# Optimization experiments

Measured on AMD Instinct MI355X. Metric: run time of the kernel, lower is better.

The kernel has to match this reference:

```python
import jax, jax.numpy as jnp
import numpy as np
import math


def setup_inputs() -> dict:
    key = jax.random.key(0)
    k0, k1, k2, k3, k4 = jax.random.split(key, 5)
    in_f, out_f, nb = 512, 512, 8
    B, S = 4, 2048
    x = jax.random.normal(k0, (B, S, in_f), dtype=jnp.float32)
    # RBF params (frozen in original: basis_trainable=False)
    fan_in = in_f  # fan_in of rbf.weight.T which is (num_basis, in_features)
    bound = 1.0 / math.sqrt(fan_in)
    rbf_weight = jax.random.uniform(k1, (in_f, nb), dtype=jnp.float32,
                                    minval=-math.sqrt(3.0) * 0.33 / math.sqrt(fan_in),
                                    maxval=math.sqrt(3.0) * 0.33 / math.sqrt(fan_in))
    rbf_centers = jnp.tile(jnp.linspace(-bound, bound, nb, dtype=jnp.float32)[None, :], (in_f, 1))
    # KAN spline weight (in, nb, out); fan_in for init is in_f*nb
    fan2 = in_f * nb
    wb = math.sqrt(3.0) * 0.33 / math.sqrt(fan2)
    weight = jax.random.uniform(k2, (in_f, nb, out_f), dtype=jnp.float32, minval=-wb, maxval=wb)
    bias = jax.random.uniform(k3, (out_f,), dtype=jnp.float32,
                              minval=-1.0 / math.sqrt(fan2), maxval=1.0 / math.sqrt(fan2))
    scale_base = jax.random.uniform(k4, (in_f, out_f), dtype=jnp.float32, minval=-0.1, maxval=0.1)
    return {"x": x, "rbf_weight": rbf_weight, "rbf_centers": rbf_centers,
            "weight": weight, "bias": bias, "scale_base": scale_base}


def reference(x, rbf_weight, rbf_centers, weight, bias, scale_base):
    in_f = x.shape[-1]
    nb = rbf_weight.shape[1]
    beta = (nb / math.log2(nb)) ** 2  # get_rbf_width(2/nb, log2(nb))
    batch_shape = x.shape[:-1]
    xf = x.reshape(-1, in_f)  # (N, in)
    # RBF basis expansion: (N, in, nb)
    z = xf[:, :, None] * rbf_weight[None, :, :] - rbf_centers[None, :, :]
    phi = jnp.exp(-beta * (z * z))
    # spline contraction + base path, expressed as efficient contractions
    y = jnp.einsum('nib,ibo->no', phi, weight)
    y = y + bias + jnp.cos(xf) @ scale_base
    return y.reshape(*batch_shape, weight.shape[-1])
```

## Files before the change

### kernel.cpp

```cpp
#include <hip/hip_runtime.h>
#include <hip/hip_bf16.h>

typedef __attribute__((ext_vector_type(8))) short short8;
typedef __attribute__((ext_vector_type(4))) float f32x4;

#define IN_F 512
#define OUT_F 512
#define BK 64
#define PHI_STEPS 64
#define NSTEPS 72
#define PAN 64
#define ACH 512
#define BCH2 2048
#define NT2 2
#define PART_ELEMS (8192 * OUT_F)
#define C2 (-10.2591705f)

__device__ __forceinline__ short f2bf(float f) {
  unsigned u = __builtin_bit_cast(unsigned, f);
  u += 0x7fffu + ((u >> 16) & 1u);
  return (short)(u >> 16);
}
__device__ __forceinline__ float b2f(unsigned short u) {
  return __builtin_bit_cast(float, (unsigned)u << 16);
}

__device__ __forceinline__ void glds16(const void* g, void* l) {
  __builtin_amdgcn_global_load_lds(
      (const __attribute__((address_space(1))) unsigned int*)g,
      (__attribute__((address_space(3))) unsigned int*)l, 16, 0, 0);
}

__device__ __forceinline__ float bsrc(const float* __restrict__ w,
                                      const float* __restrict__ sb,
                                      int k, int col) {
  return (k < IN_F * 8) ? w[(size_t)k * OUT_F + col]
                        : sb[(size_t)(k - IN_F * 8) * OUT_F + col];
}

__global__ void __launch_bounds__(256) prep_b2(const float* __restrict__ w,
                                               const float* __restrict__ sb,
                                               short* __restrict__ img) {
  const int D = blockIdx.x * 256 + threadIdx.x;
  const int ci = D & (BCH2 - 1);
  const int im = D >> 11;
  const int s = im % NSTEPS;
  const int nt = im / NSTEPS;
  const int n = ci >> 3, slot = ci & 7;
  const int oct = slot ^ (n & 7);
  const int col = nt * 256 + n;
  short8 v;
#pragma unroll
  for (int j = 0; j < 8; ++j) v[j] = f2bf(bsrc(w, sb, s * 64 + oct * 8 + j, col));
  *(short8*)&img[(size_t)D * 8] = v;
}

__global__ void __launch_bounds__(256) prep_a(const float* __restrict__ x,
                                              const float* __restrict__ rw,
                                              const float* __restrict__ rc,
                                              short* __restrict__ aimg) {
  const int D = blockIdx.x * 256 + threadIdx.x;
  const int ci = D & (ACH - 1);
  const int rest = D >> 9;
  const int s = rest % NSTEPS;
  const int pan = rest / NSTEPS;
  const int m = ci >> 3, slot = ci & 7;
  const int oct = slot ^ (m & 7);
  const int row = pan * PAN + m;
  short8 v;
  if (s < PHI_STEPS) {
    const int feat = s * 8 + oct;
    const float xv = x[(size_t)row * IN_F + feat];
    const float4 r0 = *(const float4*)(rw + feat * 8);
    const float4 r1 = *(const float4*)(rw + feat * 8 + 4);
    const float4 q0 = *(const float4*)(rc + feat * 8);
    const float4 q1 = *(const float4*)(rc + feat * 8 + 4);
    const float rwv[8] = {r0.x, r0.y, r0.z, r0.w, r1.x, r1.y, r1.z, r1.w};
    const float rcv[8] = {q0.x, q0.y, q0.z, q0.w, q1.x, q1.y, q1.z, q1.w};
#pragma unroll
    for (int j = 0; j < 8; ++j) {
      const float z = fmaf(xv, rwv[j], -rcv[j]);
      v[j] = f2bf(exp2f(C2 * z * z));
    }
  } else {
    const float* xp = x + (size_t)row * IN_F + (s - PHI_STEPS) * 64 + oct * 8;
    const float4 u0 = *(const float4*)xp, u1 = *(const float4*)(xp + 4);
    v[0] = f2bf(__cosf(u0.x)); v[1] = f2bf(__cosf(u0.y));
    v[2] = f2bf(__cosf(u0.z)); v[3] = f2bf(__cosf(u0.w));
    v[4] = f2bf(__cosf(u1.x)); v[5] = f2bf(__cosf(u1.y));
    v[6] = f2bf(__cosf(u1.z)); v[7] = f2bf(__cosf(u1.w));
  }
  *(short8*)&aimg[(size_t)D * 8] = v;
}

__global__ void __launch_bounds__(256) reduce3b(const short* __restrict__ part,
                                                float* __restrict__ out) {
  typedef __attribute__((ext_vector_type(4))) short short4v;
  const int n4 = PART_ELEMS / 4;
  const short4v* p0 = (const short4v*)part;
  const short4v* p1 = (const short4v*)(part + PART_ELEMS);
  const short4v* p2 = (const short4v*)(part + 2 * (size_t)PART_ELEMS);
  float4* o4 = (float4*)out;
  for (int i = blockIdx.x * 256 + threadIdx.x; i < n4; i += gridDim.x * 256) {
    float4 a = o4[i];
    const short4v q0 = p0[i], q1 = p1[i], q2 = p2[i];
    a.x += b2f((unsigned short)q0[0]) + b2f((unsigned short)q1[0]) + b2f((unsigned short)q2[0]);
    a.y += b2f((unsigned short)q0[1]) + b2f((unsigned short)q1[1]) + b2f((unsigned short)q2[1]);
    a.z += b2f((unsigned short)q0[2]) + b2f((unsigned short)q1[2]) + b2f((unsigned short)q2[2]);
    a.w += b2f((unsigned short)q0[3]) + b2f((unsigned short)q1[3]) + b2f((unsigned short)q2[3]);
    o4[i] = a;
  }
}

__global__ void __launch_bounds__(256) reduce_add(const float* __restrict__ part,
                                                  float* __restrict__ out) {
  const int n4 = PART_ELEMS / 4;
  const float4* p4 = (const float4*)part;
  float4* o4 = (float4*)out;
  for (int i = blockIdx.x * 256 + threadIdx.x; i < n4; i += gridDim.x * 256) {
    float4 a = o4[i];
    const float4 b = p4[i];
    a.x += b.x; a.y += b.y; a.z += b.z; a.w += b.w;
    o4[i] = a;
  }
}

__global__ void __launch_bounds__(1024, 4) kan_gemm256(
    const short* __restrict__ aimg, const short* __restrict__ bimg,
    const float* __restrict__ bias, float* __restrict__ out,
    short* __restrict__ part) {
  constexpr int SPLC = NSTEPS / 4;
  __shared__ __align__(16) short A_lds[2][256 * BK];
  __shared__ __align__(16) short B_lds[2][256 * BK];

  const int t = threadIdx.x, lane = t & 63, wid = t >> 6;
  const int wm = wid >> 2, wn = wid & 3;
  const int l15 = lane & 15, kb = lane >> 4;
  const int mb = blockIdx.x, nt = blockIdx.y;
  const int ks = blockIdx.z;
  const int m0 = mb * 256, n0 = nt * 256, s0 = ks * SPLC;

  f32x4 acc[4][4];
#pragma unroll
  for (int i = 0; i < 4; ++i)
#pragma unroll
    for (int j = 0; j < 4; ++j) acc[i][j] = (f32x4){0.f, 0.f, 0.f, 0.f};

  auto stage = [&](int s, int buf) {
#pragma unroll
    for (int c = 0; c < 2; ++c) {
      const int g = c * 1024 + t;
      const int p = g >> 9, idx = g & 511;
      const short* src = aimg + (((size_t)(4 * mb + p) * NSTEPS + s) * ACH + idx) * 8;
      glds16(src, &A_lds[buf][c * 8192 + wid * 512]);
    }
#pragma unroll
    for (int c = 0; c < 2; ++c) {
      const int g = c * 1024 + t;
      const short* src = bimg + (((size_t)nt * NSTEPS + s) * BCH2 + g) * 8;
      glds16(src, &B_lds[buf][c * 8192 + wid * 512]);
    }
  };

  auto mfma_step = [&](int buf) {
#pragma unroll
    for (int kk = 0; kk < 2; ++kk) {
      const int sk = kk * 4 + kb;
      short8 af[4], bf[4];
#pragma unroll
      for (int mi = 0; mi < 4; ++mi) {
        const int rm = mi * 16 + l15;
        af[mi] = *(const short8*)&A_lds[buf][wm * 4096 + rm * 64 + (sk ^ (rm & 7)) * 8];
      }
#pragma unroll
      for (int ni = 0; ni < 4; ++ni) {
        const int n = wn * 64 + ni * 16 + l15;
        bf[ni] = *(const short8*)&B_lds[buf][n * 64 + (sk ^ (n & 7)) * 8];
      }
#pragma unroll
      for (int mi = 0; mi < 4; ++mi)
#pragma unroll
        for (int ni = 0; ni < 4; ++ni)
          acc[mi][ni] = __builtin_amdgcn_mfma_f32_16x16x32_bf16(
              af[mi], bf[ni], acc[mi][ni], 0, 0, 0);
    }
  };

  stage(s0, 0);

  for (int si = 0; si < SPLC; ++si) {
    const int c = si & 1;
    if (si + 1 < SPLC) {
      stage(s0 + si + 1, c ^ 1);
      asm volatile("s_waitcnt vmcnt(4)" ::: "memory");
    } else {
      asm volatile("s_waitcnt vmcnt(0)" ::: "memory");
    }
    __builtin_amdgcn_s_barrier();
    mfma_step(c);
    __builtin_amdgcn_s_barrier();
  }

#pragma unroll
  for (int ni = 0; ni < 4; ++ni) {
    const int col = n0 + wn * 64 + ni * 16 + l15;
    const float bb = (ks == 0) ? bias[col] : 0.f;
#pragma unroll
    for (int mi = 0; mi < 4; ++mi) {
      const int rb = m0 + wm * 64 + mi * 16 + kb * 4;
#pragma unroll
      for (int r4 = 0; r4 < 4; ++r4) {
        const size_t idx = (size_t)(rb + r4) * OUT_F + col;
        if (ks == 0) out[idx] = acc[mi][ni][r4] + bb;
        else         part[(size_t)(ks - 1) * PART_ELEMS + idx] = f2bf(acc[mi][ni][r4]);
      }
    }
  }
}

template <int KS>
__global__ void __launch_bounds__(512, 4) kan_gemm_mid(
    const short* __restrict__ aimg, const short* __restrict__ bimg,
    const float* __restrict__ bias, float* __restrict__ out,
    float* __restrict__ part) {
  constexpr int SPLC = NSTEPS / KS;
  __shared__ __align__(16) short A_lds[2][64 * BK];
  __shared__ __align__(16) short B_lds[2][256 * BK];

  const int t = threadIdx.x, lane = t & 63, wid = t >> 6;
  const int wm = wid >> 2, wn = wid & 3;
  const int l15 = lane & 15, kb = lane >> 4;
  const int mb = blockIdx.x, nt = blockIdx.y;
  const int ks = (KS > 1) ? blockIdx.z : 0;
  const int m0 = mb * 64, n0 = nt * 256, s0 = ks * SPLC;

  f32x4 acc[2][4];
#pragma unroll
  for (int i = 0; i < 2; ++i)
#pragma unroll
    for (int j = 0; j < 4; ++j) acc[i][j] = (f32x4){0.f, 0.f, 0.f, 0.f};

  const short* abase = aimg + (size_t)mb * NSTEPS * ACH * 8;
  const short* bbase = bimg + (size_t)nt * NSTEPS * BCH2 * 8;

  auto stage = [&](int s, int buf) {
    const short* as = abase + ((size_t)s * ACH + wid * 64 + lane) * 8;
    glds16(as, &A_lds[buf][wid * 512]);
    const short* bs = bbase + ((size_t)s * BCH2 + wid * 64 + lane) * 8;
#pragma unroll
    for (int c2 = 0; c2 < 4; ++c2)
      glds16(bs + (size_t)c2 * 512 * 8, &B_lds[buf][c2 * 4096 + wid * 512]);
  };

  auto mfma_step = [&](int buf) {
#pragma unroll
    for (int kk = 0; kk < 2; ++kk) {
      const int sk = kk * 4 + kb;
      short8 af[2], bf[4];
#pragma unroll
      for (int mi = 0; mi < 2; ++mi) {
        const int r = wm * 32 + mi * 16 + l15;
        af[mi] = *(const short8*)&A_lds[buf][r * BK + (sk ^ (r & 7)) * 8];
      }
#pragma unroll
      for (int ni = 0; ni < 4; ++ni) {
        const int n = wn * 64 + ni * 16 + l15;
        bf[ni] = *(const short8*)&B_lds[buf][n * BK + (sk ^ (n & 7)) * 8];
      }
#pragma unroll
      for (int mi = 0; mi < 2; ++mi)
#pragma unroll
        for (int ni = 0; ni < 4; ++ni)
          acc[mi][ni] = __builtin_amdgcn_mfma_f32_16x16x32_bf16(
              af[mi], bf[ni], acc[mi][ni], 0, 0, 0);
    }
  };

  stage(s0, 0);
  for (int si = 0; si < SPLC; ++si) {
    const int c = si & 1;
    if (si + 1 < SPLC) {
      stage(s0 + si + 1, c ^ 1);
      asm volatile("s_waitcnt vmcnt(5)" ::: "memory");
    } else {
      asm volatile("s_waitcnt vmcnt(0)" ::: "memory");
    }
    __builtin_amdgcn_s_barrier();
    mfma_step(c);
    __builtin_amdgcn_s_barrier();
  }

#pragma unroll
  for (int ni = 0; ni < 4; ++ni) {
    const int col = n0 + wn * 64 + ni * 16 + l15;
    const float bb = (KS == 1 || ks == 0) ? bias[col] : 0.f;
#pragma unroll
    for (int mi = 0; mi < 2; ++mi) {
      const int rb = m0 + wm * 32 + mi * 16 + kb * 4;
#pragma unroll
      for (int r4 = 0; r4 < 4; ++r4) {
        const size_t idx = (size_t)(rb + r4) * OUT_F + col;
        if (KS == 1 || ks == 0) out[idx] = acc[mi][ni][r4] + bb;
        else                    part[idx] = acc[mi][ni][r4];
      }
    }
  }
}

extern "C" void kernel_launch(void* const* d_in, const int* in_sizes, int n_in,
                              void* d_out, int out_size, void* d_ws, size_t ws_size,
                              hipStream_t stream) {
  const float* x    = (const float*)d_in[0];
  const float* rw   = (const float*)d_in[1];
  const float* rc   = (const float*)d_in[2];
  const float* w    = (const float*)d_in[3];
  const float* bias = (const float*)d_in[4];
  const float* sb   = (const float*)d_in[5];
  float* out = (float*)d_out;

  const int nrows = in_sizes[0] / IN_F;
  const int npan = nrows / PAN;

  const size_t b2_bytes    = (size_t)NT2 * NSTEPS * BCH2 * 16;
  const size_t aimg_bytes  = (size_t)npan * NSTEPS * ACH * 16;
  const size_t bf16p_bytes = (size_t)3 * PART_ELEMS * sizeof(short);
  const size_t f32p_bytes  = (size_t)PART_ELEMS * sizeof(float);

  if (ws_size >= b2_bytes + aimg_bytes + bf16p_bytes) {
    short* bimg = (short*)d_ws;
    short* aimg = (short*)((char*)d_ws + b2_bytes);
    short* part = (short*)((char*)d_ws + b2_bytes + aimg_bytes);
    prep_b2<<<NT2 * NSTEPS * BCH2 / 256, 256, 0, stream>>>(w, sb, bimg);
    prep_a<<<npan * NSTEPS * ACH / 256, 256, 0, stream>>>(x, rw, rc, aimg);
    kan_gemm256<<<dim3(nrows / 256, 2, 4), 1024, 0, stream>>>(aimg, bimg, bias, out, part);
    reduce3b<<<2048, 256, 0, stream>>>(part, out);
  } else if (ws_size >= b2_bytes + aimg_bytes + f32p_bytes) {
    short* bimg = (short*)d_ws;
    short* aimg = (short*)((char*)d_ws + b2_bytes);
    float* part = (float*)((char*)d_ws + b2_bytes + aimg_bytes);
    prep_b2<<<NT2 * NSTEPS * BCH2 / 256, 256, 0, stream>>>(w, sb, bimg);
    prep_a<<<npan * NSTEPS * ACH / 256, 256, 0, stream>>>(x, rw, rc, aimg);
    kan_gemm_mid<2><<<dim3(nrows / 64, 2, 2), 512, 0, stream>>>(aimg, bimg, bias, out, part);
    reduce_add<<<2048, 256, 0, stream>>>(part, out);
  } else if (ws_size >= b2_bytes + aimg_bytes) {
    short* bimg = (short*)d_ws;
    short* aimg = (short*)((char*)d_ws + b2_bytes);
    prep_b2<<<NT2 * NSTEPS * BCH2 / 256, 256, 0, stream>>>(w, sb, bimg);
    prep_a<<<npan * NSTEPS * ACH / 256, 256, 0, stream>>>(x, rw, rc, aimg);
    kan_gemm_mid<1><<<dim3(nrows / 64, 2, 1), 512, 0, stream>>>(aimg, bimg, bias, out, nullptr);
  } else {
    short* bimg = (short*)d_ws;
    prep_b2<<<NT2 * NSTEPS * BCH2 / 256, 256, 0, stream>>>(w, sb, bimg);
    kan_gemm_mid<1><<<dim3(nrows / 64, 2, 1), 512, 0, stream>>>(nullptr, bimg, bias, out, nullptr);
  }
}
```

Measured before the change: 84.56 us.

## Restructure 256x256 GEMM into 8-wave ping-pong with quadrant-interleaved staging

Replaces the 16-wave 256x256 tile kernel with an 8-wave (512-thread) version where each wave holds a 128x64 accumulator (8x4 MFMA tiles). The K loop is split into four quadrant MFMA phases, and the half-tile A/B loads for the next steps are interleaved between them behind barriers, with s_setprio raised around the MFMA blocks. The aim is to overlap global-to-LDS transfers with matrix work and raise the MFMA-to-LDS-read ratio. In exchange it doubles accumulator registers per wave, lowers occupancy, and adds more barriers per step.

```diff
diff --git a/kernel.cpp b/kernel.cpp
--- a/kernel.cpp
+++ b/kernel.cpp
@@ -125,11 +125,11 @@
   }
 }
 
-__global__ void __launch_bounds__(1024, 4) kan_gemm256(
+__global__ void __launch_bounds__(512, 2) kan_gemm8p(
     const short* __restrict__ aimg, const short* __restrict__ bimg,
     const float* __restrict__ bias, float* __restrict__ out,
     short* __restrict__ part) {
-  constexpr int SPLC = NSTEPS / 4;
+  constexpr int KT = NSTEPS / 4;
   __shared__ __align__(16) short A_lds[2][256 * BK];
   __shared__ __align__(16) short B_lds[2][256 * BK];
 
@@ -138,81 +138,103 @@
   const int l15 = lane & 15, kb = lane >> 4;
   const int mb = blockIdx.x, nt = blockIdx.y;
   const int ks = blockIdx.z;
-  const int m0 = mb * 256, n0 = nt * 256, s0 = ks * SPLC;
-
-  f32x4 acc[4][4];
-#pragma unroll
-  for (int i = 0; i < 4; ++i)
+  const int m0 = mb * 256, n0 = nt * 256, s0 = ks * KT;
+
+  f32x4 acc[8][4];
+#pragma unroll
+  for (int i = 0; i < 8; ++i)
 #pragma unroll
     for (int j = 0; j < 4; ++j) acc[i][j] = (f32x4){0.f, 0.f, 0.f, 0.f};
 
-  auto stage = [&](int s, int buf) {
-#pragma unroll
-    for (int c = 0; c < 2; ++c) {
-      const int g = c * 1024 + t;
-      const int p = g >> 9, idx = g & 511;
-      const short* src = aimg + (((size_t)(4 * mb + p) * NSTEPS + s) * ACH + idx) * 8;
-      glds16(src, &A_lds[buf][c * 8192 + wid * 512]);
-    }
-#pragma unroll
-    for (int c = 0; c < 2; ++c) {
-      const int g = c * 1024 + t;
-      const short* src = bimg + (((size_t)nt * NSTEPS + s) * BCH2 + g) * 8;
-      glds16(src, &B_lds[buf][c * 8192 + wid * 512]);
-    }
-  };
-
-  auto mfma_step = [&](int buf) {
+  auto stageA = [&](int kt, int h, int buf) {
+#pragma unroll
+    for (int j = 0; j < 2; ++j) {
+      const int wi = wid * 2 + j;
+      const int pr = wi >> 3, seg = wi & 7;
+      const int pan = 4 * mb + h + pr * 2;
+      const short* src = aimg + (((size_t)pan * NSTEPS + kt) * ACH + seg * 64 + lane) * 8;
+      glds16(src, &A_lds[buf][((h + pr * 2) * 512 + seg * 64) * 8]);
+    }
+  };
+  auto stageB = [&](int kt, int h, int buf) {
+#pragma unroll
+    for (int j = 0; j < 2; ++j) {
+      const int wi = wid * 2 + j;
+      const int r = wi >> 2, sg = wi & 3;
+      const int cb = h * 256 + r * 512 + sg * 64;
+      const short* src = bimg + (((size_t)nt * NSTEPS + kt) * BCH2 + cb + lane) * 8;
+      glds16(src, &B_lds[buf][cb * 8]);
+    }
+  };
+
+  auto quad = [&](int buf, int qr, int qc) {
 #pragma unroll
     for (int kk = 0; kk < 2; ++kk) {
       const int sk = kk * 4 + kb;
-      short8 af[4], bf[4];
+      short8 af[4], bf[2];
 #pragma unroll
       for (int mi = 0; mi < 4; ++mi) {
-        const int rm = mi * 16 + l15;
-        af[mi] = *(const short8*)&A_lds[buf][wm * 4096 + rm * 64 + (sk ^ (rm & 7)) * 8];
-      }
-#pragma unroll
-      for (int ni = 0; ni < 4; ++ni) {
-        const int n = wn * 64 + ni * 16 + l15;
+        const int r = wm * 128 + (qr * 4 + mi) * 16 + l15;
+        af[mi] = *(const short8*)&A_lds[buf][r * 64 + (sk ^ (r & 7)) * 8];
+      }
+#pragma unroll
+      for (int ni = 0; ni < 2; ++ni) {
+        const int n = wn * 64 + (qc * 2 + ni) * 16 + l15;
         bf[ni] = *(const short8*)&B_lds[buf][n * 64 + (sk ^ (n & 7)) * 8];
       }
 #pragma unroll
       for (int mi = 0; mi < 4; ++mi)
 #pragma unroll
-        for (int ni = 0; ni < 4; ++ni)
-          acc[mi][ni] = __builtin_amdgcn_mfma_f32_16x16x32_bf16(
-              af[mi], bf[ni], acc[mi][ni], 0, 0, 0);
-    }
-  };
-
-  stage(s0, 0);
-
-  for (int si = 0; si < SPLC; ++si) {
-    const int c = si & 1;
-    if (si + 1 < SPLC) {
-      stage(s0 + si + 1, c ^ 1);
-      asm volatile("s_waitcnt vmcnt(4)" ::: "memory");
-    } else {
-      asm volatile("s_waitcnt vmcnt(0)" ::: "memory");
-    }
-    __builtin_amdgcn_s_barrier();
-    mfma_step(c);
-    __builtin_amdgcn_s_barrier();
-  }
-
-#pragma unroll
-  for (int ni = 0; ni < 4; ++ni) {
-    const int col = n0 + wn * 64 + ni * 16 + l15;
+        for (int ni = 0; ni < 2; ++ni)
+          acc[qr * 4 + mi][qc * 2 + ni] = __builtin_amdgcn_mfma_f32_16x16x32_bf16(
+              af[mi], bf[ni], acc[qr * 4 + mi][qc * 2 + ni], 0, 0, 0);
+    }
+  };
+
+  stageA(s0, 0, 0);     stageB(s0, 0, 0);
+  stageA(s0, 1, 0);     stageB(s0, 1, 0);
+  stageA(s0 + 1, 0, 1); stageB(s0 + 1, 0, 1);
+
+  for (int tl = 0; tl < KT; ++tl) {
+    const int b = tl & 1;
+    const int kt = s0 + tl;
+    if (tl + 1 < KT) stageA(kt + 1, 1, b ^ 1);
+    if (tl < KT - 1) { asm volatile("s_waitcnt vmcnt(6)" ::: "memory"); }
+    else             { asm volatile("s_waitcnt vmcnt(0)" ::: "memory"); }
+    __builtin_amdgcn_s_barrier();
+    __builtin_amdgcn_s_setprio(1);
+    quad(b, 0, 0);
+    __builtin_amdgcn_s_setprio(0);
+    __builtin_amdgcn_s_barrier();
+    if (tl + 1 < KT) stageB(kt + 1, 1, b ^ 1);
+    __builtin_amdgcn_s_setprio(1);
+    quad(b, 0, 1);
+    __builtin_amdgcn_s_setprio(0);
+    __builtin_amdgcn_s_barrier();
+    if (tl + 2 < KT) stageA(kt + 2, 0, b);
+    __builtin_amdgcn_s_setprio(1);
+    quad(b, 1, 0);
+    __builtin_amdgcn_s_setprio(0);
+    __builtin_amdgcn_s_barrier();
+    if (tl + 2 < KT) stageB(kt + 2, 0, b);
+    __builtin_amdgcn_s_setprio(1);
+    quad(b, 1, 1);
+    __builtin_amdgcn_s_setprio(0);
+    __builtin_amdgcn_s_barrier();
+  }
+
+#pragma unroll
+  for (int fj = 0; fj < 4; ++fj) {
+    const int col = n0 + wn * 64 + fj * 16 + l15;
     const float bb = (ks == 0) ? bias[col] : 0.f;
 #pragma unroll
-    for (int mi = 0; mi < 4; ++mi) {
-      const int rb = m0 + wm * 64 + mi * 16 + kb * 4;
+    for (int fi = 0; fi < 8; ++fi) {
+      const int rb = m0 + wm * 128 + fi * 16 + kb * 4;
 #pragma unroll
       for (int r4 = 0; r4 < 4; ++r4) {
         const size_t idx = (size_t)(rb + r4) * OUT_F + col;
-        if (ks == 0) out[idx] = acc[mi][ni][r4] + bb;
-        else         part[(size_t)(ks - 1) * PART_ELEMS + idx] = f2bf(acc[mi][ni][r4]);
+        if (ks == 0) out[idx] = acc[fi][fj][r4] + bb;
+        else         part[(size_t)(ks - 1) * PART_ELEMS + idx] = f2bf(acc[fi][fj][r4]);
       }
     }
   }
@@ -332,7 +354,7 @@
     short* part = (short*)((char*)d_ws + b2_bytes + aimg_bytes);
     prep_b2<<<NT2 * NSTEPS * BCH2 / 256, 256, 0, stream>>>(w, sb, bimg);
     prep_a<<<npan * NSTEPS * ACH / 256, 256, 0, stream>>>(x, rw, rc, aimg);
-    kan_gemm256<<<dim3(nrows / 256, 2, 4), 1024, 0, stream>>>(aimg, bimg, bias, out, part);
+    kan_gemm8p<<<dim3(nrows / 256, 2, 4), 512, 0, stream>>>(aimg, bimg, bias, out, part);
     reduce3b<<<2048, 256, 0, stream>>>(part, out);
   } else if (ws_size >= b2_bytes + aimg_bytes + f32p_bytes) {
     short* bimg = (short*)d_ws;
```

New measurement: 111.5 us. 1.32x slower.

## Load B fragments directly to registers in fragment order, skipping LDS

Applied to the files above, without the earlier changes.

Adds a prep kernel that writes the weight image in MFMA-fragment order, so each lane in the main GEMM loads its B operands straight from global memory into registers, double-buffered across K steps. Only A is still staged through LDS. The block shrinks from 1024 to 512 threads, and each wave now computes 128x64 outputs with 32 accumulators. This halves LDS traffic and footprint, but raises register pressure and makes each wave wait on per-lane global B loads.

```diff
diff --git a/kernel.cpp b/kernel.cpp
--- a/kernel.cpp
+++ b/kernel.cpp
@@ -36,6 +36,25 @@
                                       int k, int col) {
   return (k < IN_F * 8) ? w[(size_t)k * OUT_F + col]
                         : sb[(size_t)(k - IN_F * 8) * OUT_F + col];
+}
+
+__global__ void __launch_bounds__(256) prep_bf(const float* __restrict__ w,
+                                               const float* __restrict__ sb,
+                                               short* __restrict__ img) {
+  const int D = blockIdx.x * 256 + threadIdx.x;
+  const int ci = D & (BCH2 - 1);
+  const int im = D >> 11;
+  const int s = im % NSTEPS;
+  const int nt = im / NSTEPS;
+  const int lane = ci & 63;
+  const int kk = (ci >> 6) & 1;
+  const int c = ci >> 7;
+  const int col = nt * 256 + c * 16 + (lane & 15);
+  const int kbase = s * 64 + (kk * 4 + (lane >> 4)) * 8;
+  short8 v;
+#pragma unroll
+  for (int j = 0; j < 8; ++j) v[j] = f2bf(bsrc(w, sb, kbase + j, col));
+  *(short8*)&img[(size_t)D * 8] = v;
 }
 
 __global__ void __launch_bounds__(256) prep_b2(const float* __restrict__ w,
@@ -125,94 +144,108 @@
   }
 }
 
-__global__ void __launch_bounds__(1024, 4) kan_gemm256(
-    const short* __restrict__ aimg, const short* __restrict__ bimg,
+__device__ __forceinline__ f32x4 MFMA(short8 a, short8 b, f32x4 c) {
+  return __builtin_amdgcn_mfma_f32_16x16x32_bf16(a, b, c, 0, 0, 0);
+}
+
+__global__ void __launch_bounds__(512, 2) kan_gemm_bd(
+    const short* __restrict__ aimg, const short* __restrict__ bfimg,
     const float* __restrict__ bias, float* __restrict__ out,
     short* __restrict__ part) {
-  constexpr int SPLC = NSTEPS / 4;
+  constexpr int KT = NSTEPS / 4;
   __shared__ __align__(16) short A_lds[2][256 * BK];
-  __shared__ __align__(16) short B_lds[2][256 * BK];
 
   const int t = threadIdx.x, lane = t & 63, wid = t >> 6;
   const int wm = wid >> 2, wn = wid & 3;
   const int l15 = lane & 15, kb = lane >> 4;
   const int mb = blockIdx.x, nt = blockIdx.y;
   const int ks = blockIdx.z;
-  const int m0 = mb * 256, n0 = nt * 256, s0 = ks * SPLC;
-
-  f32x4 acc[4][4];
-#pragma unroll
-  for (int i = 0; i < 4; ++i)
+  const int m0 = mb * 256, n0 = nt * 256, s0 = ks * KT;
+
+  f32x4 acc[8][4];
+#pragma unroll
+  for (int i = 0; i < 8; ++i)
 #pragma unroll
     for (int j = 0; j < 4; ++j) acc[i][j] = (f32x4){0.f, 0.f, 0.f, 0.f};
 
-  auto stage = [&](int s, int buf) {
-#pragma unroll
-    for (int c = 0; c < 2; ++c) {
-      const int g = c * 1024 + t;
-      const int p = g >> 9, idx = g & 511;
-      const short* src = aimg + (((size_t)(4 * mb + p) * NSTEPS + s) * ACH + idx) * 8;
-      glds16(src, &A_lds[buf][c * 8192 + wid * 512]);
-    }
-#pragma unroll
-    for (int c = 0; c < 2; ++c) {
-      const int g = c * 1024 + t;
-      const short* src = bimg + (((size_t)nt * NSTEPS + s) * BCH2 + g) * 8;
-      glds16(src, &B_lds[buf][c * 8192 + wid * 512]);
-    }
-  };
-
-  auto mfma_step = [&](int buf) {
+  const short* bfbase = bfimg + (size_t)nt * NSTEPS * BCH2 * 8;
+
+  auto stageA = [&](int kt, int buf) {
+#pragma unroll
+    for (int c = 0; c < 4; ++c) {
+      const short* src = aimg +
+          (((size_t)(4 * mb + c) * NSTEPS + kt) * ACH + wid * 64 + lane) * 8;
+      glds16(src, &A_lds[buf][(c * 512 + wid * 64) * 8]);
+    }
+  };
+
+  auto loadB = [&](int kt, short8* Bs) {
+    const short* base = bfbase + (size_t)kt * BCH2 * 8;
+#pragma unroll
+    for (int kk = 0; kk < 2; ++kk)
+#pragma unroll
+      for (int fj = 0; fj < 4; ++fj)
+        Bs[kk * 4 + fj] =
+            *(const short8*)&base[((((wn * 4 + fj) * 2 + kk) * 64) + lane) * 8];
+  };
+
+  auto mma_tile = [&](const short* __restrict__ Ab, const short8* Bs) {
 #pragma unroll
     for (int kk = 0; kk < 2; ++kk) {
       const int sk = kk * 4 + kb;
-      short8 af[4], bf[4];
-#pragma unroll
-      for (int mi = 0; mi < 4; ++mi) {
-        const int rm = mi * 16 + l15;
-        af[mi] = *(const short8*)&A_lds[buf][wm * 4096 + rm * 64 + (sk ^ (rm & 7)) * 8];
-      }
-#pragma unroll
-      for (int ni = 0; ni < 4; ++ni) {
-        const int n = wn * 64 + ni * 16 + l15;
-        bf[ni] = *(const short8*)&B_lds[buf][n * 64 + (sk ^ (n & 7)) * 8];
-      }
-#pragma unroll
-      for (int mi = 0; mi < 4; ++mi)
-#pragma unroll
-        for (int ni = 0; ni < 4; ++ni)
-          acc[mi][ni] = __builtin_amdgcn_mfma_f32_16x16x32_bf16(
-              af[mi], bf[ni], acc[mi][ni], 0, 0, 0);
-    }
-  };
-
-  stage(s0, 0);
-
-  for (int si = 0; si < SPLC; ++si) {
-    const int c = si & 1;
-    if (si + 1 < SPLC) {
-      stage(s0 + si + 1, c ^ 1);
-      asm volatile("s_waitcnt vmcnt(4)" ::: "memory");
-    } else {
-      asm volatile("s_waitcnt vmcnt(0)" ::: "memory");
-    }
-    __builtin_amdgcn_s_barrier();
-    mfma_step(c);
-    __builtin_amdgcn_s_barrier();
-  }
-
-#pragma unroll
-  for (int ni = 0; ni < 4; ++ni) {
-    const int col = n0 + wn * 64 + ni * 16 + l15;
+      short8 af[8];
+#pragma unroll
+      for (int fi = 0; fi < 8; ++fi) {
+        const int r = wm * 128 + fi * 16 + l15;
+        af[fi] = *(const short8*)&Ab[r * 64 + (sk ^ (r & 7)) * 8];
+      }
+#pragma unroll
+      for (int fi = 0; fi < 8; ++fi)
+#pragma unroll
+        for (int fj = 0; fj < 4; ++fj)
+          acc[fi][fj] = MFMA(af[fi], Bs[kk * 4 + fj], acc[fi][fj]);
+    }
+  };
+
+  short8 B0[8], B1[8];
+
+  stageA(s0, 0);
+  loadB(s0, B0);
+
+#define KAN_TILE(TL, BCUR, BNXT)                                              \
+  {                                                                           \
+    const int tl = (TL);                                                      \
+    const int b = tl & 1;                                                     \
+    if (tl + 1 < KT) {                                                        \
+      stageA(s0 + tl + 1, b ^ 1);                                             \
+      loadB(s0 + tl + 1, BNXT);                                               \
+      asm volatile("s_waitcnt vmcnt(12)" ::: "memory");                       \
+    } else {                                                                  \
+      asm volatile("s_waitcnt vmcnt(0)" ::: "memory");                        \
+    }                                                                         \
+    __builtin_amdgcn_s_barrier();                                             \
+    mma_tile(&A_lds[b][0], BCUR);                                             \
+    __builtin_amdgcn_s_barrier();                                             \
+  }
+
+  for (int tt = 0; tt < KT; tt += 2) {
+    KAN_TILE(tt, B0, B1)
+    KAN_TILE(tt + 1, B1, B0)
+  }
+#undef KAN_TILE
+
+#pragma unroll
+  for (int fj = 0; fj < 4; ++fj) {
+    const int col = n0 + wn * 64 + fj * 16 + l15;
     const float bb = (ks == 0) ? bias[col] : 0.f;
 #pragma unroll
-    for (int mi = 0; mi < 4; ++mi) {
-      const int rb = m0 + wm * 64 + mi * 16 + kb * 4;
+    for (int fi = 0; fi < 8; ++fi) {
+      const int rb = m0 + wm * 128 + fi * 16 + kb * 4;
 #pragma unroll
       for (int r4 = 0; r4 < 4; ++r4) {
         const size_t idx = (size_t)(rb + r4) * OUT_F + col;
-        if (ks == 0) out[idx] = acc[mi][ni][r4] + bb;
-        else         part[(size_t)(ks - 1) * PART_ELEMS + idx] = f2bf(acc[mi][ni][r4]);
+        if (ks == 0) out[idx] = acc[fi][fj][r4] + bb;
+        else         part[(size_t)(ks - 1) * PART_ELEMS + idx] = f2bf(acc[fi][fj][r4]);
       }
     }
   }
@@ -271,8 +304,7 @@
       for (int mi = 0; mi < 2; ++mi)
 #pragma unroll
         for (int ni = 0; ni < 4; ++ni)
-          acc[mi][ni] = __builtin_amdgcn_mfma_f32_16x16x32_bf16(
-              af[mi], bf[ni], acc[mi][ni], 0, 0, 0);
+          acc[mi][ni] = MFMA(af[mi], bf[ni], acc[mi][ni]);
     }
   };
 
@@ -321,36 +353,37 @@
   const int nrows = in_sizes[0] / IN_F;
   const int npan = nrows / PAN;
 
-  const size_t b2_bytes    = (size_t)NT2 * NSTEPS * BCH2 * 16;
+  const size_t b_bytes     = (size_t)NT2 * NSTEPS * BCH2 * 16;
   const size_t aimg_bytes  = (size_t)npan * NSTEPS * ACH * 16;
   const size_t bf16p_bytes = (size_t)3 * PART_ELEMS * sizeof(short);
   const size_t f32p_bytes  = (size_t)PART_ELEMS * sizeof(float);
-
-  if (ws_size >= b2_bytes + aimg_bytes + bf16p_bytes) {
+  const int bch_total = NT2 * NSTEPS * BCH2;
+
+  if (ws_size >= b_bytes + aimg_bytes + bf16p_bytes) {
     short* bimg = (short*)d_ws;
-    short* aimg = (short*)((char*)d_ws + b2_bytes);
-    short* part = (short*)((char*)d_ws + b2_bytes + aimg_bytes);
-    prep_b2<<<NT2 * NSTEPS * BCH2 / 256, 256, 0, stream>>>(w, sb, bimg);
+    short* aimg = (short*)((char*)d_ws + b_bytes);
+    short* part = (short*)((char*)d_ws + b_bytes + aimg_bytes);
+    prep_bf<<<bch_total / 256, 256, 0, stream>>>(w, sb, bimg);
     prep_a<<<npan * NSTEPS * ACH / 256, 256, 0, stream>>>(x, rw, rc, aimg);
-    kan_gemm256<<<dim3(nrows / 256, 2, 4), 1024, 0, stream>>>(aimg, bimg, bias, out, part);
+    kan_gemm_bd<<<dim3(nrows / 256, 2, 4), 512, 0, stream>>>(aimg, bimg, bias, out, part);
     reduce3b<<<2048, 256, 0, stream>>>(part, out);
-  } else if (ws_size >= b2_bytes + aimg_bytes + f32p_bytes) {
+  } else if (ws_size >= b_bytes + aimg_bytes + f32p_bytes) {
     short* bimg = (short*)d_ws;
-    short* aimg = (short*)((char*)d_ws + b2_bytes);
-    float* part = (float*)((char*)d_ws + b2_bytes + aimg_bytes);
-    prep_b2<<<NT2 * NSTEPS * BCH2 / 256, 256, 0, stream>>>(w, sb, bimg);
+    short* aimg = (short*)((char*)d_ws + b_bytes);
+    float* part = (float*)((char*)d_ws + b_bytes + aimg_bytes);
+    prep_b2<<<bch_total / 256, 256, 0, stream>>>(w, sb, bimg);
     prep_a<<<npan * NSTEPS * ACH / 256, 256, 0, stream>>>(x, rw, rc, aimg);
     kan_gemm_mid<2><<<dim3(nrows / 64, 2, 2), 512, 0, stream>>>(aimg, bimg, bias, out, part);
     reduce_add<<<2048, 256, 0, stream>>>(part, out);
-  } else if (ws_size >= b2_bytes + aimg_bytes) {
+  } else if (ws_size >= b_bytes + aimg_bytes) {
     short* bimg = (short*)d_ws;
-    short* aimg = (short*)((char*)d_ws + b2_bytes);
-    prep_b2<<<NT2 * NSTEPS * BCH2 / 256, 256, 0, stream>>>(w, sb, bimg);
+    short* aimg = (short*)((char*)d_ws + b_bytes);
+    prep_b2<<<bch_total / 256, 256, 0, stream>>>(w, sb, bimg);
     prep_a<<<npan * NSTEPS * ACH / 256, 256, 0, stream>>>(x, rw, rc, aimg);
     kan_gemm_mid<1><<<dim3(nrows / 64, 2, 1), 512, 0, stream>>>(aimg, bimg, bias, out, nullptr);
   } else {
     short* bimg = (short*)d_ws;
-    prep_b2<<<NT2 * NSTEPS * BCH2 / 256, 256, 0, stream>>>(w, sb, bimg);
+    prep_b2<<<bch_total / 256, 256, 0, stream>>>(w, sb, bimg);
     kan_gemm_mid<1><<<dim3(nrows / 64, 2, 1), 512, 0, stream>>>(nullptr, bimg, bias, out, nullptr);
   }
 }
```

Result: slower. 113.8 us (+34.5%).
